# Performance work log

Hardware: AMD Instinct MI355X
Metric: run time of the kernel (lower is better)

Reference implementation:

```python
import jax, jax.numpy as jnp
import numpy as np

M, N = 128, 128          # SOM grid
NITER = 1000             # total training iterations
ALPHA = 0.3              # base learning rate (torch default)
SIGMA = max(M, N) / 2.0  # base neighbourhood radius (torch default)
BS, DIM = 4096, 768


def setup_inputs() -> dict:
    key = jax.random.key(0)
    k1, k2 = jax.random.split(key)
    embedded = jax.random.normal(k1, (BS, DIM), dtype=jnp.float32)   # SapBERT CLS reps
    weights = jax.random.normal(k2, (M * N, DIM), dtype=jnp.float32)  # codebook / SOM weights
    return {"embedded": embedded, "weights": weights, "it": 100}


def reference(embedded, weights, it):
    comps = weights.shape[0]
    # neuron grid locations [comps, 2] (row-major i,j like neuron_locations())
    locs = jnp.stack(
        jnp.meshgrid(jnp.arange(M), jnp.arange(N), indexing="ij"), axis=-1
    ).reshape(comps, 2).astype(jnp.float32)

    # BMU search: squared Euclidean distances (argmin identical to argmin of sqrt)
    # [bs, comps] — avoids materializing the torch [bs, comps, dim] repeat
    d2 = (
        jnp.sum(embedded * embedded, axis=1)[:, None]
        + jnp.sum(weights * weights, axis=1)[None, :]
        - 2.0 * (embedded @ weights.T)
    )
    bmu_index = jnp.argmin(d2, axis=1)          # [bs]
    bmu_loc = locs[bmu_index]                   # [bs, 2] gather

    # linearly decaying learning rate / sigma
    decay = 1.0 - it / NITER
    alpha_op = ALPHA * decay
    sigma_op = SIGMA * decay

    # Gaussian neighbourhood over grid distances [bs, comps]
    grid_d2 = jnp.sum((locs[None, :, :] - bmu_loc[:, None, :]) ** 2, axis=-1)
    lr = alpha_op * jnp.exp(-grid_d2 / (sigma_op * sigma_op))

    # delta[c,d] = sum_b lr[b,c] * (x[b,d] - w[c,d])  (no bs x comps x dim materialization)
    delta = jnp.einsum("bc,bd->cd", lr, embedded) - jnp.sum(lr, axis=0)[:, None] * weights
    return weights + delta
```

## Files before the change

kernel.cpp:

```cpp
#include <hip/hip_runtime.h>
#include <cstdint>
#include <cstddef>

#define BS    4096
#define DIM   768
#define GM    128
#define GN    128
#define COMPS (GM * GN)
#define NITER_F 1000.0f
#define ALPHA0  0.3f
#define SIGMA0  64.0f

typedef _Float16 half8  __attribute__((ext_vector_type(8)));
typedef _Float16 half4v __attribute__((ext_vector_type(4)));
typedef float    floatx4 __attribute__((ext_vector_type(4)));

#define XH_OFF    0UL
#define WH_OFF    (8UL * 1024UL * 1024UL)
#define G_OFF     0UL
#define G_BYTES   ((size_t)COMPS * DIM * 4UL)
#define BEST_OFF  G_BYTES
#define BEST_BYTES ((size_t)BS * 8UL)
#define CNT_OFF   (BEST_OFF + BEST_BYTES)
#define CNT_BYTES ((size_t)COMPS * 4UL)
#define WN2_OFF   (CNT_OFF + CNT_BYTES)

#define GPTR(p) ((const __attribute__((address_space(1))) void*)(p))
#define LPTR(p) ((__attribute__((address_space(3))) void*)(p))

__device__ __forceinline__ unsigned long long packScore(float s, int c) {
    unsigned u = __float_as_uint(s);
    u = (u & 0x80000000u) ? ~u : (u | 0x80000000u);
    return ((unsigned long long)u << 32) | (unsigned)(~(unsigned)c);
}

__device__ __forceinline__ unsigned long long shfl_xor_u64(unsigned long long v, int m) {
    unsigned lo = (unsigned)v, hi = (unsigned)(v >> 32);
    lo = (unsigned)__shfl_xor((int)lo, m, 64);
    hi = (unsigned)__shfl_xor((int)hi, m, 64);
    return ((unsigned long long)hi << 32) | lo;
}

__global__ void cvt_kernel(const float* __restrict__ src, _Float16* __restrict__ dst, int n4) {
    int i = blockIdx.x * 256 + threadIdx.x;
    if (i >= n4) return;
    float4 v = ((const float4*)src)[i];
    half4v h;
    h[0] = (_Float16)v.x; h[1] = (_Float16)v.y;
    h[2] = (_Float16)v.z; h[3] = (_Float16)v.w;
    ((half4v*)dst)[i] = h;
}

__global__ __launch_bounds__(192) void cvtw_wn2_kernel(
    const float* __restrict__ w, _Float16* __restrict__ wh, float* __restrict__ wn2) {
    const int c = blockIdx.x;
    const int t = threadIdx.x;
    const size_t i4 = (size_t)c * 192 + t;
    float4 v = ((const float4*)w)[i4];
    half4v h;
    h[0] = (_Float16)v.x; h[1] = (_Float16)v.y;
    h[2] = (_Float16)v.z; h[3] = (_Float16)v.w;
    ((half4v*)wh)[i4] = h;
    float s = v.x * v.x + v.y * v.y + v.z * v.z + v.w * v.w;
    #pragma unroll
    for (int off = 32; off; off >>= 1) s += __shfl_down(s, off, 64);
    __shared__ float p[3];
    if ((t & 63) == 0) p[t >> 6] = s;
    __syncthreads();
    if (t == 0) wn2[c] = 0.5f * (p[0] + p[1] + p[2]);
}

#define BMU_NT 24

__global__ __launch_bounds__(512, 2) void bmu_kernel(
    const _Float16* __restrict__ xh, const _Float16* __restrict__ wh,
    const float* __restrict__ wn2, unsigned long long* __restrict__ best) {
    __shared__ _Float16 AB[4][2][8192];
    __shared__ unsigned long long red[256];

    const int tid  = threadIdx.x;
    const int wv   = tid >> 6;
    const int lane = tid & 63;
    const int l15  = lane & 15;
    const int q    = lane >> 4;
    const int wr   = wv >> 2;
    const int wc   = wv & 3;

    const int bid = blockIdx.x;
    const int xcd = bid & 7;
    const int rem = bid >> 3;
    const int bb  = rem & 15;
    const int cb  = xcd * 8 + (rem >> 4);
    const int b0 = bb * 256;
    const int c0 = cb * 256;

    if (tid < 256) red[tid] = 0ULL;

    const int Ls = tid >> 3;
    const int ss = tid & 7;
    const int sl = ss ^ (Ls & 7);
    const int prow = 2 * Ls + (sl >> 2);
    const int kc8  = (sl & 3) * 8;
    const _Float16* gA0 = xh + (size_t)(b0 + prow) * DIM + kc8;
    const _Float16* gA1 = gA0 + (size_t)128 * DIM;
    const _Float16* gB0 = wh + (size_t)(c0 + prow) * DIM + kc8;
    const _Float16* gB1 = gB0 + (size_t)128 * DIM;
    const int ldsoff = wv * 512;

    int aoff[8], boff[4];
    #pragma unroll
    for (int i = 0; i < 8; ++i) {
        const int row = wr * 128 + i * 16 + l15;
        const int line = row >> 1;
        const int ps = (((row & 1) << 2) | q) ^ (line & 7);
        aoff[i] = line * 64 + ps * 8;
    }
    #pragma unroll
    for (int jj = 0; jj < 4; ++jj) {
        const int row = wc * 64 + jj * 16 + l15;
        const int line = row >> 1;
        const int ps = (((row & 1) << 2) | q) ^ (line & 7);
        boff[jj] = line * 64 + ps * 8;
    }

    floatx4 acc[8][4];
    #pragma unroll
    for (int i = 0; i < 8; ++i)
        #pragma unroll
        for (int jj = 0; jj < 4; ++jj) acc[i][jj] = (floatx4){0.f, 0.f, 0.f, 0.f};

    #pragma unroll
    for (int t = 0; t < 3; ++t) {
        _Float16* A = &AB[t][0][0];
        _Float16* B = &AB[t][1][0];
        __builtin_amdgcn_global_load_lds(GPTR(gA0 + t * 32), LPTR(A + ldsoff),        16, 0, 0);
        __builtin_amdgcn_global_load_lds(GPTR(gA1 + t * 32), LPTR(A + 4096 + ldsoff), 16, 0, 0);
        __builtin_amdgcn_global_load_lds(GPTR(gB0 + t * 32), LPTR(B + ldsoff),        16, 0, 0);
        __builtin_amdgcn_global_load_lds(GPTR(gB1 + t * 32), LPTR(B + 4096 + ldsoff), 16, 0, 0);
    }

    for (int t = 0; t < BMU_NT; ++t) {
        if (t < BMU_NT - 2)       asm volatile("s_waitcnt vmcnt(8)" ::: "memory");
        else if (t == BMU_NT - 2) asm volatile("s_waitcnt vmcnt(4)" ::: "memory");
        else                      asm volatile("s_waitcnt vmcnt(0)" ::: "memory");
        __builtin_amdgcn_s_barrier();
        asm volatile("" ::: "memory");

        const _Float16* A = &AB[t & 3][0][0];
        const _Float16* B = &AB[t & 3][1][0];
        const bool more = (t + 3) < BMU_NT;
        _Float16* An = &AB[(t + 3) & 3][0][0];
        _Float16* Bn = &AB[(t + 3) & 3][1][0];
        const int t3 = (t + 3) * 32;

        half8 af[8], bf[4];
        #pragma unroll
        for (int i = 0; i < 4; ++i) af[i] = *(const half8*)(A + aoff[i]);
        bf[0] = *(const half8*)(B + boff[0]);
        bf[1] = *(const half8*)(B + boff[1]);
        if (more) __builtin_amdgcn_global_load_lds(GPTR(gA0 + t3), LPTR(An + ldsoff), 16, 0, 0);
        __builtin_amdgcn_s_setprio(1);
        #pragma unroll
        for (int i = 0; i < 4; ++i) {
            acc[i][0] = __builtin_amdgcn_mfma_f32_16x16x32_f16(af[i], bf[0], acc[i][0], 0, 0, 0);
            acc[i][1] = __builtin_amdgcn_mfma_f32_16x16x32_f16(af[i], bf[1], acc[i][1], 0, 0, 0);
        }
        __builtin_amdgcn_s_setprio(0);
        #pragma unroll
        for (int i = 4; i < 8; ++i) af[i] = *(const half8*)(A + aoff[i]);
        if (more) __builtin_amdgcn_global_load_lds(GPTR(gA1 + t3), LPTR(An + 4096 + ldsoff), 16, 0, 0);
        __builtin_amdgcn_s_setprio(1);
        #pragma unroll
        for (int i = 4; i < 8; ++i) {
            acc[i][0] = __builtin_amdgcn_mfma_f32_16x16x32_f16(af[i], bf[0], acc[i][0], 0, 0, 0);
            acc[i][1] = __builtin_amdgcn_mfma_f32_16x16x32_f16(af[i], bf[1], acc[i][1], 0, 0, 0);
        }
        __builtin_amdgcn_s_setprio(0);
        bf[2] = *(const half8*)(B + boff[2]);
        bf[3] = *(const half8*)(B + boff[3]);
        if (more) __builtin_amdgcn_global_load_lds(GPTR(gB0 + t3), LPTR(Bn + ldsoff), 16, 0, 0);
        __builtin_amdgcn_s_setprio(1);
        #pragma unroll
        for (int i = 4; i < 8; ++i) {
            acc[i][2] = __builtin_amdgcn_mfma_f32_16x16x32_f16(af[i], bf[2], acc[i][2], 0, 0, 0);
            acc[i][3] = __builtin_amdgcn_mfma_f32_16x16x32_f16(af[i], bf[3], acc[i][3], 0, 0, 0);
        }
        __builtin_amdgcn_s_setprio(0);
        if (more) __builtin_amdgcn_global_load_lds(GPTR(gB1 + t3), LPTR(Bn + 4096 + ldsoff), 16, 0, 0);
        __builtin_amdgcn_s_setprio(1);
        #pragma unroll
        for (int i = 0; i < 4; ++i) {
            acc[i][2] = __builtin_amdgcn_mfma_f32_16x16x32_f16(af[i], bf[2], acc[i][2], 0, 0, 0);
            acc[i][3] = __builtin_amdgcn_mfma_f32_16x16x32_f16(af[i], bf[3], acc[i][3], 0, 0, 0);
        }
        __builtin_amdgcn_s_setprio(0);
    }

    float wnj[4];
    #pragma unroll
    for (int jj = 0; jj < 4; ++jj) wnj[jj] = wn2[c0 + wc * 64 + jj * 16 + l15];

    #pragma unroll
    for (int i = 0; i < 8; ++i) {
        #pragma unroll
        for (int r = 0; r < 4; ++r) {
            unsigned long long m = 0ULL;
            #pragma unroll
            for (int jj = 0; jj < 4; ++jj) {
                const float s = acc[i][jj][r] - wnj[jj];
                const unsigned long long p = packScore(s, c0 + wc * 64 + jj * 16 + l15);
                if (p > m) m = p;
            }
            #pragma unroll
            for (int msk = 1; msk <= 8; msk <<= 1) {
                const unsigned long long o = shfl_xor_u64(m, msk);
                if (o > m) m = o;
            }
            if (l15 == 0)
                atomicMax(&red[wr * 128 + i * 16 + q * 4 + r], m);
        }
    }
    __syncthreads();
    if (tid < 256) atomicMax(&best[b0 + tid], red[tid]);
}

__global__ void scatter_kernel(const unsigned long long* __restrict__ best,
                               const float* __restrict__ x,
                               float* __restrict__ G, float* __restrict__ cnt) {
    const int b = blockIdx.x;
    const int c = (int)(~(unsigned)(best[b] & 0xFFFFFFFFULL));
    float* gr = G + (size_t)c * DIM;
    const float* xr = x + (size_t)b * DIM;
    #pragma unroll
    for (int u = 0; u < 3; ++u) {
        const int d = threadIdx.x + u * 256;
        atomicAdd(&gr[d], xr[d]);
    }
    if (threadIdx.x == 0) atomicAdd(&cnt[c], 1.0f);
}

#define EP 136
#define BP 40

__global__ __launch_bounds__(256) void convA_kernel(
    const float* G, _Float16* Hh, const int* __restrict__ itp) {
    __shared__ _Float16 Es[128 * EP];
    __shared__ _Float16 Bs[128 * BP];
    const int d0 = blockIdx.x * 128;
    const int ib = blockIdx.y;
    const int tid = threadIdx.x;
    const int wv = tid >> 6, lane = tid & 63;
    const int l15 = lane & 15, q = lane >> 4;
    const int mrow = (wv >> 1) * 64, ncol = (wv & 1) * 64;

    {
        const float decay = 1.f - (float)(*itp) / NITER_F;
        const float sig = SIGMA0 * decay;
        const float inv = -1.f / (sig * sig);
        const int row = tid >> 1, hh = tid & 1;
        _Float16* dst = Es + row * EP + hh * 64;
        #pragma unroll
        for (int u = 0; u < 64; ++u) {
            const float dd = (float)(row - hh * 64 - u);
            dst[u] = (_Float16)__expf(dd * dd * inv);
        }
    }

    floatx4 acc[4][4];
    #pragma unroll
    for (int i = 0; i < 4; ++i)
        #pragma unroll
        for (int j = 0; j < 4; ++j) acc[i][j] = (floatx4){0.f, 0.f, 0.f, 0.f};

    const int dpo = (tid & 15) * 8;
    const int rsel = tid >> 4;
    for (int k0 = 0; k0 < 128; k0 += 32) {
        __syncthreads();
        #pragma unroll
        for (int s = 0; s < 2; ++s) {
            const int j = k0 + s * 16 + rsel;
            const float* r = G + (size_t)(ib * 128 + j) * DIM + d0 + dpo;
            float4 a0 = *(const float4*)r, a1 = *(const float4*)(r + 4);
            float va[8] = {a0.x, a0.y, a0.z, a0.w, a1.x, a1.y, a1.z, a1.w};
            #pragma unroll
            for (int u = 0; u < 8; ++u)
                Bs[(dpo + u) * BP + (s * 16 + rsel)] = (_Float16)va[u];
        }
        __syncthreads();
        half8 af[4], bf[4];
        #pragma unroll
        for (int i = 0; i < 4; ++i)
            af[i] = *(const half8*)(Es + (mrow + i * 16 + l15) * EP + k0 + q * 8);
        #pragma unroll
        for (int j = 0; j < 4; ++j)
            bf[j] = *(const half8*)(Bs + (ncol + j * 16 + l15) * BP + q * 8);
        #pragma unroll
        for (int i = 0; i < 4; ++i)
            #pragma unroll
            for (int j = 0; j < 4; ++j)
                acc[i][j] = __builtin_amdgcn_mfma_f32_16x16x32_f16(af[i], bf[j], acc[i][j], 0, 0, 0);
    }
    __syncthreads();
    float* Ebf = (float*)Es;
    #pragma unroll
    for (int ch = 0; ch < 2; ++ch) {
        if ((wv >> 1) == ch) {
            #pragma unroll
            for (int i = 0; i < 4; ++i)
                #pragma unroll
                for (int j = 0; j < 4; ++j)
                    #pragma unroll
                    for (int r = 0; r < 4; ++r)
                        Ebf[(i * 16 + q * 4 + r) * 132 + ncol + j * 16 + l15] = acc[i][j][r];
        }
        __syncthreads();
        {
            const int row = tid >> 2, seg = tid & 3;
            const int m = ch * 64 + row;
            _Float16* hp = Hh + (size_t)(ib * 128 + m) * 1536 + d0 * 2 + seg * 32;
            #pragma unroll
            for (int u = 0; u < 4; ++u) {
                const float* sp = Ebf + row * 132 + seg * 32 + u * 8;
                half8 hv;
                #pragma unroll
                for (int e = 0; e < 8; ++e) hv[e] = (_Float16)sp[e];
                *(half8*)(hp + u * 8) = hv;
            }
        }
        __syncthreads();
    }
}

__global__ __launch_bounds__(256) void convB_kernel(
    const _Float16* Hh, const float* __restrict__ w, const float* __restrict__ cnt,
    const int* __restrict__ itp, float* __restrict__ out) {
    __shared__ _Float16 Es[128 * EP];
    __shared__ _Float16 Bs[128 * BP];
    __shared__ float cntHs[128];
    __shared__ float Ss[128];
    const int d0 = blockIdx.x * 128;
    const int jc = blockIdx.y;
    const int tid = threadIdx.x;
    const int wv = tid >> 6, lane = tid & 63;
    const int l15 = lane & 15, q = lane >> 4;
    const int mrow = (wv >> 1) * 64, ncol = (wv & 1) * 64;
    const float decay = 1.f - (float)(*itp) / NITER_F;
    const float alpha = ALPHA0 * decay;
    const float sig = SIGMA0 * decay;
    const float inv = -1.f / (sig * sig);

    if (tid < 128) {
        float s = 0.f;
        for (int j = 0; j < 128; ++j) {
            const float dd = (float)(jc - j);
            s += __expf(dd * dd * inv) * cnt[tid * 128 + j];
        }
        cntHs[tid] = s;
    }
    {
        const int row = tid >> 1, hh = tid & 1;
        _Float16* dst = Es + row * EP + hh * 64;
        #pragma unroll
        for (int u = 0; u < 64; ++u) {
            const float dd = (float)(row - hh * 64 - u);
            dst[u] = (_Float16)__expf(dd * dd * inv);
        }
    }
    __syncthreads();
    if (tid < 128) {
        float s = 0.f;
        for (int i = 0; i < 128; ++i) {
            const float dd = (float)(tid - i);
            s += __expf(dd * dd * inv) * cntHs[i];
        }
        Ss[tid] = s;
    }

    floatx4 acc[4][4];
    #pragma unroll
    for (int i = 0; i < 4; ++i)
        #pragma unroll
        for (int j = 0; j < 4; ++j) acc[i][j] = (floatx4){0.f, 0.f, 0.f, 0.f};

    const int dpo = (tid & 15) * 8;
    const int rsel = tid >> 4;
    for (int k0 = 0; k0 < 128; k0 += 32) {
        __syncthreads();
        #pragma unroll
        for (int s = 0; s < 2; ++s) {
            const int i = k0 + s * 16 + rsel;
            const half8 v = *(const half8*)(Hh + (size_t)(i * 128 + jc) * 1536 + d0 * 2 + dpo);
            #pragma unroll
            for (int u = 0; u < 8; ++u)
                Bs[(dpo + u) * BP + (s * 16 + rsel)] = v[u];
        }
        __syncthreads();
        half8 af[4], bf[4];
        #pragma unroll
        for (int i = 0; i < 4; ++i)
            af[i] = *(const half8*)(Es + (mrow + i * 16 + l15) * EP + k0 + q * 8);
        #pragma unroll
        for (int j = 0; j < 4; ++j)
            bf[j] = *(const half8*)(Bs + (ncol + j * 16 + l15) * BP + q * 8);
        #pragma unroll
        for (int i = 0; i < 4; ++i)
            #pragma unroll
            for (int j = 0; j < 4; ++j)
                acc[i][j] = __builtin_amdgcn_mfma_f32_16x16x32_f16(af[i], bf[j], acc[i][j], 0, 0, 0);
    }
    __syncthreads();
    float* Ebf = (float*)Es;
    #pragma unroll
    for (int ch = 0; ch < 2; ++ch) {
        if ((wv >> 1) == ch) {
            #pragma unroll
            for (int i = 0; i < 4; ++i)
                #pragma unroll
                for (int j = 0; j < 4; ++j)
                    #pragma unroll
                    for (int r = 0; r < 4; ++r)
                        Ebf[(i * 16 + q * 4 + r) * 132 + ncol + j * 16 + l15] = acc[i][j][r];
        }
        __syncthreads();
        {
            const int row = tid >> 2, seg = tid & 3;
            const int m = ch * 64 + row;
            const int c = m * 128 + jc;
            const float scl = 1.f - alpha * Ss[m];
            const size_t g = (size_t)c * DIM + d0 + seg * 32;
            #pragma unroll
            for (int u = 0; u < 8; ++u) {
                float4 wv4 = *(const float4*)(w + g + u * 4);
                float4 t4  = *(const float4*)(Ebf + row * 132 + seg * 32 + u * 4);
                float4 o;
                o.x = wv4.x * scl + alpha * t4.x;
                o.y = wv4.y * scl + alpha * t4.y;
                o.z = wv4.z * scl + alpha * t4.z;
                o.w = wv4.w * scl + alpha * t4.w;
                *(float4*)(out + g + u * 4) = o;
            }
        }
        __syncthreads();
    }
}

extern "C" void kernel_launch(void* const* d_in, const int* in_sizes, int n_in,
                              void* d_out, int out_size, void* d_ws, size_t ws_size,
                              hipStream_t stream) {
    const float* x  = (const float*)d_in[0];
    const float* w  = (const float*)d_in[1];
    const int* itp  = (const int*)d_in[2];
    float* out = (float*)d_out;
    char* ws = (char*)d_ws;

    _Float16* xh = (_Float16*)(ws + XH_OFF);
    _Float16* wh = (_Float16*)(ws + WH_OFF);
    float*    G  = (float*)(ws + G_OFF);
    _Float16* Hh = (_Float16*)(ws + G_OFF);
    unsigned long long* best = (unsigned long long*)(ws + BEST_OFF);
    float* cnt  = (float*)(ws + CNT_OFF);
    float* wn2  = (float*)(ws + WN2_OFF);

    hipMemsetAsync(ws + BEST_OFF, 0, BEST_BYTES + CNT_BYTES, stream);

    cvt_kernel<<<(BS * DIM / 4 + 255) / 256, 256, 0, stream>>>(x, xh, BS * DIM / 4);
    cvtw_wn2_kernel<<<COMPS, 192, 0, stream>>>(w, wh, wn2);

    bmu_kernel<<<dim3(1024), 512, 0, stream>>>(xh, wh, wn2, best);

    hipMemsetAsync(ws + G_OFF, 0, G_BYTES, stream);
    scatter_kernel<<<BS, 256, 0, stream>>>(best, x, G, cnt);

    convA_kernel<<<dim3(6, 128), 256, 0, stream>>>(G, Hh, itp);
    convB_kernel<<<dim3(6, 128), 256, 0, stream>>>(Hh, w, cnt, itp, out);
}
```

Baseline: 332.2 us.

## Restructure BMU GEMM main loop into two-phase barrier ping-pong and remap block tiles

Rewrites the BMU GEMM K-loop into two half-phases, each with its own barrier. In the first phase all eight A fragments plus half the B fragments are loaded and the A prefetch is issued. In the second phase the remaining B fragments and B prefetch follow, with the vmcnt wait moved to the end of the iteration. Scheduling barriers and setprio wrap long MFMA bursts, aiming for better overlap of LDS reads, global prefetch and matrix math across co-resident waves. It also reorders the block-to-tile mapping so consecutive blocks on an XCD share groups of four weight column blocks, for better L2 reuse; this adds more barriers per iteration and more live fragment registers.

```diff
diff --git a/kernel.cpp b/kernel.cpp
--- a/kernel.cpp
+++ b/kernel.cpp
@@ -89,8 +89,10 @@
     const int bid = blockIdx.x;
     const int xcd = bid & 7;
     const int rem = bid >> 3;
-    const int bb  = rem & 15;
-    const int cb  = xcd * 8 + (rem >> 4);
+    const int cbl = rem & 3;
+    const int bb  = (rem >> 2) & 15;
+    const int cbg = rem >> 6;
+    const int cb  = xcd * 8 + cbg * 4 + cbl;
     const int b0 = bb * 256;
     const int c0 = cb * 256;
 
@@ -138,14 +140,10 @@
         __builtin_amdgcn_global_load_lds(GPTR(gB0 + t * 32), LPTR(B + ldsoff),        16, 0, 0);
         __builtin_amdgcn_global_load_lds(GPTR(gB1 + t * 32), LPTR(B + 4096 + ldsoff), 16, 0, 0);
     }
+    asm volatile("s_waitcnt vmcnt(8)" ::: "memory");
+    __builtin_amdgcn_s_barrier();
 
     for (int t = 0; t < BMU_NT; ++t) {
-        if (t < BMU_NT - 2)       asm volatile("s_waitcnt vmcnt(8)" ::: "memory");
-        else if (t == BMU_NT - 2) asm volatile("s_waitcnt vmcnt(4)" ::: "memory");
-        else                      asm volatile("s_waitcnt vmcnt(0)" ::: "memory");
-        __builtin_amdgcn_s_barrier();
-        asm volatile("" ::: "memory");
-
         const _Float16* A = &AB[t & 3][0][0];
         const _Float16* B = &AB[t & 3][1][0];
         const bool more = (t + 3) < BMU_NT;
@@ -155,45 +153,49 @@
 
         half8 af[8], bf[4];
         #pragma unroll
-        for (int i = 0; i < 4; ++i) af[i] = *(const half8*)(A + aoff[i]);
+        for (int i = 0; i < 8; ++i) af[i] = *(const half8*)(A + aoff[i]);
         bf[0] = *(const half8*)(B + boff[0]);
         bf[1] = *(const half8*)(B + boff[1]);
-        if (more) __builtin_amdgcn_global_load_lds(GPTR(gA0 + t3), LPTR(An + ldsoff), 16, 0, 0);
+        if (more) {
+            __builtin_amdgcn_global_load_lds(GPTR(gA0 + t3), LPTR(An + ldsoff),        16, 0, 0);
+            __builtin_amdgcn_global_load_lds(GPTR(gA1 + t3), LPTR(An + 4096 + ldsoff), 16, 0, 0);
+        }
+        __builtin_amdgcn_sched_barrier(0);
+        __builtin_amdgcn_s_barrier();
+        asm volatile("s_waitcnt lgkmcnt(0)" ::: "memory");
+        __builtin_amdgcn_sched_barrier(0);
         __builtin_amdgcn_s_setprio(1);
         #pragma unroll
-        for (int i = 0; i < 4; ++i) {
+        for (int i = 0; i < 8; ++i) {
             acc[i][0] = __builtin_amdgcn_mfma_f32_16x16x32_f16(af[i], bf[0], acc[i][0], 0, 0, 0);
             acc[i][1] = __builtin_amdgcn_mfma_f32_16x16x32_f16(af[i], bf[1], acc[i][1], 0, 0, 0);
         }
         __builtin_amdgcn_s_setprio(0);
-        #pragma unroll
-        for (int i = 4; i < 8; ++i) af[i] = *(const half8*)(A + aoff[i]);
-        if (more) __builtin_amdgcn_global_load_lds(GPTR(gA1 + t3), LPTR(An + 4096 + ldsoff), 16, 0, 0);
-        __builtin_amdgcn_s_setprio(1);
-        #pragma unroll
-        for (int i = 4; i < 8; ++i) {
-            acc[i][0] = __builtin_amdgcn_mfma_f32_16x16x32_f16(af[i], bf[0], acc[i][0], 0, 0, 0);
-            acc[i][1] = __builtin_amdgcn_mfma_f32_16x16x32_f16(af[i], bf[1], acc[i][1], 0, 0, 0);
-        }
-        __builtin_amdgcn_s_setprio(0);
+        __builtin_amdgcn_sched_barrier(0);
+        __builtin_amdgcn_s_barrier();
+
         bf[2] = *(const half8*)(B + boff[2]);
         bf[3] = *(const half8*)(B + boff[3]);
-        if (more) __builtin_amdgcn_global_load_lds(GPTR(gB0 + t3), LPTR(Bn + ldsoff), 16, 0, 0);
+        if (more) {
+            __builtin_amdgcn_global_load_lds(GPTR(gB0 + t3), LPTR(Bn + ldsoff),        16, 0, 0);
+            __builtin_amdgcn_global_load_lds(GPTR(gB1 + t3), LPTR(Bn + 4096 + ldsoff), 16, 0, 0);
+        }
+        if (t < BMU_NT - 3)       asm volatile("s_waitcnt vmcnt(8)" ::: "memory");
+        else if (t == BMU_NT - 3) asm volatile("s_waitcnt vmcnt(4)" ::: "memory");
+        else                      asm volatile("s_waitcnt vmcnt(0)" ::: "memory");
+        __builtin_amdgcn_sched_barrier(0);
+        __builtin_amdgcn_s_barrier();
+        asm volatile("s_waitcnt lgkmcnt(0)" ::: "memory");
+        __builtin_amdgcn_sched_barrier(0);
         __builtin_amdgcn_s_setprio(1);
         #pragma unroll
-        for (int i = 4; i < 8; ++i) {
+        for (int i = 0; i < 8; ++i) {
             acc[i][2] = __builtin_amdgcn_mfma_f32_16x16x32_f16(af[i], bf[2], acc[i][2], 0, 0, 0);
             acc[i][3] = __builtin_amdgcn_mfma_f32_16x16x32_f16(af[i], bf[3], acc[i][3], 0, 0, 0);
         }
         __builtin_amdgcn_s_setprio(0);
-        if (more) __builtin_amdgcn_global_load_lds(GPTR(gB1 + t3), LPTR(Bn + 4096 + ldsoff), 16, 0, 0);
-        __builtin_amdgcn_s_setprio(1);
-        #pragma unroll
-        for (int i = 0; i < 4; ++i) {
-            acc[i][2] = __builtin_amdgcn_mfma_f32_16x16x32_f16(af[i], bf[2], acc[i][2], 0, 0, 0);
-            acc[i][3] = __builtin_amdgcn_mfma_f32_16x16x32_f16(af[i], bf[3], acc[i][3], 0, 0, 0);
-        }
-        __builtin_amdgcn_s_setprio(0);
+        __builtin_amdgcn_sched_barrier(0);
+        __builtin_amdgcn_s_barrier();
     }
 
     float wnj[4];
```

Result: slower. 341.7 us (+2.9%).
